# Kernel optimization log

Measured on AMD Instinct MI355X. Metric: run time of the kernel, lower is better.

## Reference

```python
import jax, jax.numpy as jnp
import numpy as np

N, E, D, R, L = 50000, 600000, 64, 65, 2


def setup_inputs() -> dict:
    key = jax.random.key(0)
    ks = jax.random.split(key, 10)
    x = jax.random.normal(ks[0], (N, D), dtype=jnp.float32)
    edge_index = jax.random.randint(ks[1], (2, E), 0, N, dtype=jnp.int64)
    edge_type = jax.random.randint(ks[2], (E,), 0, R, dtype=jnp.int64)
    s = 1.0 / np.sqrt(D)
    W = jax.random.normal(ks[3], (L, R, D, D), dtype=jnp.float32) * s
    root = jax.random.normal(ks[4], (L, D, D), dtype=jnp.float32) * s
    bias = jax.random.normal(ks[5], (L, D), dtype=jnp.float32) * 0.01
    res_W = jax.random.normal(ks[6], (L, D, D), dtype=jnp.float32) * s
    res_b = jax.random.normal(ks[7], (L, D), dtype=jnp.float32) * 0.01
    return {"x": x, "edge_index": edge_index, "edge_type": edge_type,
            "W": W, "root": root, "bias": bias, "res_W": res_W, "res_b": res_b}


def _rgcn_conv(x, src, dst, edge_type, W_r, W_root, b):
    # PyG RGCNConv (num_bases=None, aggr='mean'):
    #   out_i = x_i @ W_root + b + sum_r mean_{j in N_r(i)} (x_j @ W_r)
    # mean is linear, so aggregate raw features per (node, relation) first,
    # then apply the per-relation transform once per node.
    n, d = x.shape
    r = W_r.shape[0]
    seg = dst * r + edge_type                       # [E]
    msg = x[src]                                    # [E, D] gather
    agg = jax.ops.segment_sum(msg, seg, num_segments=n * r).reshape(n, r, d)
    cnt = jax.ops.segment_sum(jnp.ones((msg.shape[0],), x.dtype), seg,
                              num_segments=n * r).reshape(n, r, 1)
    mean = agg / jnp.maximum(cnt, 1.0)              # [N, R, D]
    out = jnp.einsum('nrd,rdk->nk', mean, W_r)
    return out + x @ W_root + b


def reference(x, edge_index, edge_type, W, root, bias, res_W, res_b):
    src, dst = edge_index[0], edge_index[1]
    h = x
    for l in range(W.shape[0]):
        conv = _rgcn_conv(h, src, dst, edge_type, W[l], root[l], bias[l])
        conv = jax.nn.relu(conv)
        # dropout: identity in eval mode
        res = jax.nn.relu(h @ res_W[l] + res_b[l])
        h = conv + res
    return h
```

## Files before the change

kernel.cpp:

```cpp
#include <hip/hip_runtime.h>


constexpr int NN  = 50000;
constexpr int EE  = 600000;
constexpr int DIM = 64;
constexpr int RR  = 65;
constexpr int CHUNK = 256;
constexpr int MAXCHUNKS = EE / CHUNK + RR + 8;
constexpr int SORT_BS = 2048;
constexpr int NSB = (EE + SORT_BS - 1) / SORT_BS;
constexpr int SCAN_BS = 1024;
constexpr int SCAN_NB = (NN + SCAN_BS - 1) / SCAN_BS;
constexpr int XNB = 64;

typedef __attribute__((ext_vector_type(8))) short short8v;
typedef __attribute__((ext_vector_type(4))) float floatx4;

__device__ inline unsigned short f2bf(float f) {
  unsigned int u = __float_as_uint(f);
  return (unsigned short)((u + 0x7fffu + ((u >> 16) & 1u)) >> 16);
}
__device__ inline float bf2f(unsigned short v) {
  return __uint_as_float(((unsigned int)v) << 16);
}


__global__ __launch_bounds__(256) void zero4_k(int4* __restrict__ p, int n4) {
  const int i = blockIdx.x * 256 + threadIdx.x;
  if (i < n4) p[i] = make_int4(0, 0, 0, 0);
}

__global__ __launch_bounds__(512) void cnt_k(const int* __restrict__ dst,
                                             const int* __restrict__ et,
                                             int* __restrict__ cnt, int E) {
  const int e = blockIdx.x * 512 + threadIdx.x;
  if (e < E) atomicAdd(&cnt[et[e] * NN + dst[e]], 1);
}

__global__ __launch_bounds__(512) void bhist_k(const int* __restrict__ et,
                                               int* __restrict__ bhist, int E) {
  __shared__ int lh[RR];
  if (threadIdx.x < RR) lh[threadIdx.x] = 0;
  __syncthreads();
  const int base = blockIdx.x * SORT_BS;
#pragma unroll
  for (int it = 0; it < SORT_BS / 512; ++it) {
    const int e = base + it * 512 + threadIdx.x;
    if (e < E) atomicAdd(&lh[et[e]], 1);
  }
  __syncthreads();
  if (threadIdx.x < RR) bhist[blockIdx.x * RR + threadIdx.x] = lh[threadIdx.x];
}


__global__ __launch_bounds__(1024) void scan1_k(const int* __restrict__ cnt,
                                                int* __restrict__ deg,
                                                int* __restrict__ bsum) {
  __shared__ int s[SCAN_BS];
  const int idx = blockIdx.x * SCAN_BS + threadIdx.x;
  int d = 0;
  if (idx < NN) {
#pragma unroll 13
    for (int r = 0; r < RR; ++r) d += cnt[r * NN + idx];
    deg[idx] = d;
  }
  s[threadIdx.x] = d;
  __syncthreads();
  for (int off = SCAN_BS / 2; off > 0; off >>= 1) {
    if (threadIdx.x < off) s[threadIdx.x] += s[threadIdx.x + off];
    __syncthreads();
  }
  if (threadIdx.x == 0) bsum[blockIdx.x] = s[0];
}

__global__ __launch_bounds__(64) void scan2_k(int* __restrict__ bsum) {
  if (threadIdx.x == 0) {
    int run = 0;
    for (int b = 0; b < SCAN_NB; ++b) { const int v = bsum[b]; bsum[b] = run; run += v; }
  }
}

__global__ __launch_bounds__(1024) void scan3_k(const int* __restrict__ deg,
                                                const int* __restrict__ bsum,
                                                int* __restrict__ rowptr,
                                                int* __restrict__ poscur) {
  __shared__ int s[SCAN_BS];
  const int t = threadIdx.x;
  const int idx = blockIdx.x * SCAN_BS + t;
  const int v = (idx < NN) ? deg[idx] : 0;
  s[t] = v;
  __syncthreads();
  for (int off = 1; off < SCAN_BS; off <<= 1) {
    const int u = (t >= off) ? s[t - off] : 0;
    __syncthreads();
    s[t] += u;
    __syncthreads();
  }
  const int excl = bsum[blockIdx.x] + s[t] - v;
  if (idx < NN) { rowptr[idx] = excl; poscur[idx] = excl; }
  if (idx == NN - 1) rowptr[NN] = EE;
}


__global__ __launch_bounds__(512) void scan_rel_k(const int* __restrict__ bhist,
                                                  int* __restrict__ boffrel,
                                                  int* __restrict__ total) {
  __shared__ int s[512];
  const int r = blockIdx.x;
  const int t = threadIdx.x;
  const int v = (t < NSB) ? bhist[t * RR + r] : 0;
  s[t] = v;
  __syncthreads();
  for (int off = 1; off < 512; off <<= 1) {
    const int u = (t >= off) ? s[t - off] : 0;
    __syncthreads();
    s[t] += u;
    __syncthreads();
  }
  if (t < NSB) boffrel[t * RR + r] = s[t] - v;
  if (t == 511) total[r] = s[511];
}

__global__ __launch_bounds__(128) void scan_tot_k(const int* __restrict__ total,
                                                  int* __restrict__ tptrg,
                                                  int4* __restrict__ chunkArr,
                                                  int* __restrict__ nchunks) {
  __shared__ int tptr[RR + 1], chbase[RR + 1];
  const int t = threadIdx.x;
  if (t == 0) {
    int run = 0, crun = 0;
    for (int r = 0; r < RR; ++r) {
      tptr[r] = run;    run  += total[r];
      chbase[r] = crun; crun += (total[r] + CHUNK - 1) / CHUNK;
    }
    tptr[RR] = run; chbase[RR] = crun;
    *nchunks = crun;
  }
  __syncthreads();
  if (t < RR) {
    tptrg[t] = tptr[t];
    const int tot = total[t];
    const int nc = (tot + CHUNK - 1) / CHUNK;
    for (int i = 0; i < nc; ++i) {
      const int beg = tptr[t] + i * CHUNK;
      chunkArr[chbase[t] + i] = make_int4(beg, min(beg + CHUNK, tptr[t] + tot), t, 0);
    }
  }
}

__global__ __launch_bounds__(512) void scatter_k(const int* __restrict__ src,
                                                 const int* __restrict__ dst,
                                                 const int* __restrict__ et,
                                                 const int* __restrict__ cnt,
                                                 const int* __restrict__ boffrel,
                                                 const int* __restrict__ tptrg,
                                                 int* __restrict__ poscur,
                                                 int* __restrict__ osrc,
                                                 int* __restrict__ opos,
                                                 float* __restrict__ oscale, int E) {
  __shared__ int cur[RR];
  if (threadIdx.x < RR)
    cur[threadIdx.x] = tptrg[threadIdx.x] + boffrel[blockIdx.x * RR + threadIdx.x];
  __syncthreads();
  const int base = blockIdx.x * SORT_BS;
#pragma unroll
  for (int it = 0; it < SORT_BS / 512; ++it) {
    const int e = base + it * 512 + threadIdx.x;
    if (e < E) {
      const int s = src[e], d = dst[e], r = et[e];
      const int q = atomicAdd(&cur[r], 1);
      const int p = atomicAdd(&poscur[d], 1);
      osrc[q] = s;
      opos[q] = p;
      oscale[q] = 1.0f / (float)cnt[r * NN + d];
    }
  }
}


__global__ __launch_bounds__(256) void cvtw_k(const float* __restrict__ W,
                                              unsigned short* __restrict__ WT) {
  const int tid = blockIdx.x * 256 + threadIdx.x;
  const int total4 = 2 * RR * DIM * DIM / 4;
  if (tid >= total4) return;
  const int base = tid * 4;
  const int mat = base >> 12;
  const int rem = base & 4095;
  const int k = rem >> 6, c0 = rem & 63;
  const float4 v = *reinterpret_cast<const float4*>(W + base);
  unsigned short* o = WT + (size_t)mat * 4096;
  o[(c0 + 0) * 64 + k] = f2bf(v.x);
  o[(c0 + 1) * 64 + k] = f2bf(v.y);
  o[(c0 + 2) * 64 + k] = f2bf(v.z);
  o[(c0 + 3) * 64 + k] = f2bf(v.w);
}


__global__ __launch_bounds__(256) void msgm_k(const unsigned short* __restrict__ hbf,
                                              const int* __restrict__ osrc,
                                              const int* __restrict__ opos,
                                              const float* __restrict__ oscale,
                                              const unsigned short* __restrict__ WT,
                                              const int4* __restrict__ chunkArr,
                                              const int* __restrict__ nchunks,
                                              unsigned short* __restrict__ m) {
  const int ci = blockIdx.x;
  if (ci >= *nchunks) return;
  const int4 c = chunkArr[ci];
  const int beg = c.x, end = c.y, rel = c.z;

  __shared__ unsigned short Wl[DIM][72];
  {
    const float4* s4 = reinterpret_cast<const float4*>(WT + (size_t)rel * 4096);
#pragma unroll
    for (int it = 0; it < 2; ++it) {
      const int seg = threadIdx.x + it * 256;
      const int row = seg >> 3, s8 = seg & 7;
      *reinterpret_cast<float4*>(&Wl[row][s8 * 8]) = s4[seg];
    }
  }
  __syncthreads();

  const int w  = threadIdx.x >> 6;
  const int l  = threadIdx.x & 63;
  const int lr = l & 15, lq = l >> 4;

  const int ebase = beg + w * 64;
  if (ebase >= end) return;

  short8v a[4][2];
#pragma unroll
  for (int ct = 0; ct < 4; ++ct)
#pragma unroll
    for (int kk = 0; kk < 2; ++kk)
      a[ct][kk] = *reinterpret_cast<const short8v*>(&Wl[ct * 16 + lr][kk * 32 + lq * 8]);

  short8v b[4][2];
  int eidx[4];
#pragma unroll
  for (int et = 0; et < 4; ++et) {
    eidx[et] = ebase + et * 16 + lr;
    const int e = min(eidx[et], end - 1);
    const int s = osrc[e];
    const unsigned short* hp = hbf + (size_t)s * DIM;
    b[et][0] = *reinterpret_cast<const short8v*>(hp + lq * 8);
    b[et][1] = *reinterpret_cast<const short8v*>(hp + 32 + lq * 8);
  }

  floatx4 acc[4][4];
#pragma unroll
  for (int ct = 0; ct < 4; ++ct)
#pragma unroll
    for (int et = 0; et < 4; ++et)
      acc[ct][et] = (floatx4){0.f, 0.f, 0.f, 0.f};

#pragma unroll
  for (int kk = 0; kk < 2; ++kk)
#pragma unroll
    for (int ct = 0; ct < 4; ++ct)
#pragma unroll
      for (int et = 0; et < 4; ++et)
        acc[ct][et] = __builtin_amdgcn_mfma_f32_16x16x32_bf16(a[ct][kk], b[et][kk],
                                                              acc[ct][et], 0, 0, 0);

#pragma unroll
  for (int et = 0; et < 4; ++et) {
    const int e = eidx[et];
    if (e < end) {
      const float sc = oscale[e];
      unsigned short* op = m + (size_t)opos[e] * DIM;
#pragma unroll
      for (int ct = 0; ct < 4; ++ct) {
        ushort4 o;
        o.x = f2bf(acc[ct][et][0] * sc);
        o.y = f2bf(acc[ct][et][1] * sc);
        o.z = f2bf(acc[ct][et][2] * sc);
        o.w = f2bf(acc[ct][et][3] * sc);
        *reinterpret_cast<ushort4*>(op + ct * 16 + lq * 4) = o;
      }
    }
  }
}

__global__ __launch_bounds__(256) void xform_k(const float* __restrict__ h,
                                               const float* __restrict__ root,
                                               const float* __restrict__ bias,
                                               const float* __restrict__ rw,
                                               const float* __restrict__ rb,
                                               float* __restrict__ rt,
                                               float* __restrict__ rs,
                                               unsigned short* __restrict__ hbf, int N) {
  __shared__ float Wl0[DIM * DIM];
  __shared__ float Wl1[DIM * DIM];
  __shared__ float xs[XNB][68];
#pragma unroll
  for (int i = 0; i < 4; ++i) {
    reinterpret_cast<float4*>(Wl0)[threadIdx.x + i * 256] =
        reinterpret_cast<const float4*>(root)[threadIdx.x + i * 256];
    reinterpret_cast<float4*>(Wl1)[threadIdx.x + i * 256] =
        reinterpret_cast<const float4*>(rw)[threadIdx.x + i * 256];
  }

  const int g = threadIdx.x >> 4, li = threadIdx.x & 15;
  const int base = blockIdx.x * XNB;
#pragma unroll
  for (int r = 0; r < 4; ++r) {
    const int n = base + g * 4 + r;
    float4 v = make_float4(0.f, 0.f, 0.f, 0.f);
    if (n < N) v = *reinterpret_cast<const float4*>(h + (size_t)n * DIM + li * 4);
    *reinterpret_cast<float4*>(&xs[g * 4 + r][li * 4]) = v;
  }
  __syncthreads();

  if (hbf != nullptr) {
#pragma unroll
    for (int r = 0; r < 4; ++r) {
      const int n = base + g * 4 + r;
      if (n < N) {
        const float4 v = *reinterpret_cast<const float4*>(&xs[g * 4 + r][li * 4]);
        ushort4 o;
        o.x = f2bf(v.x); o.y = f2bf(v.y); o.z = f2bf(v.z); o.w = f2bf(v.w);
        *reinterpret_cast<ushort4*>(hbf + (size_t)n * DIM + li * 4) = o;
      }
    }
  }

  float aR[4][4], aS[4][4];
#pragma unroll
  for (int r = 0; r < 4; ++r)
#pragma unroll
    for (int q = 0; q < 4; ++q) { aR[r][q] = 0.f; aS[r][q] = 0.f; }

#pragma unroll 4
  for (int k = 0; k < DIM; ++k) {
    const float4 wr = *reinterpret_cast<const float4*>(&Wl0[k * DIM + li * 4]);
    const float4 wv = *reinterpret_cast<const float4*>(&Wl1[k * DIM + li * 4]);
#pragma unroll
    for (int r = 0; r < 4; ++r) {
      const float xv = xs[g * 4 + r][k];
      aR[r][0] += xv * wr.x; aR[r][1] += xv * wr.y; aR[r][2] += xv * wr.z; aR[r][3] += xv * wr.w;
      aS[r][0] += xv * wv.x; aS[r][1] += xv * wv.y; aS[r][2] += xv * wv.z; aS[r][3] += xv * wv.w;
    }
  }

  const float4 bv = reinterpret_cast<const float4*>(bias)[li];
  const float4 cv = reinterpret_cast<const float4*>(rb)[li];
#pragma unroll
  for (int r = 0; r < 4; ++r) {
    const int n = base + g * 4 + r;
    if (n < N) {
      *reinterpret_cast<float4*>(rt + (size_t)n * DIM + li * 4) =
          make_float4(aR[r][0] + bv.x, aR[r][1] + bv.y, aR[r][2] + bv.z, aR[r][3] + bv.w);
      *reinterpret_cast<float4*>(rs + (size_t)n * DIM + li * 4) =
          make_float4(fmaxf(aS[r][0] + cv.x, 0.f), fmaxf(aS[r][1] + cv.y, 0.f),
                      fmaxf(aS[r][2] + cv.z, 0.f), fmaxf(aS[r][3] + cv.w, 0.f));
    }
  }
}

__global__ __launch_bounds__(256) void gather2_k(const unsigned short* __restrict__ m,
                                                 const int* __restrict__ rowptr,
                                                 const float* __restrict__ rt,
                                                 const float* __restrict__ rs,
                                                 float* __restrict__ hout, int N) {
  const int g = threadIdx.x >> 4, li = threadIdx.x & 15;
  const int n = blockIdx.x * 16 + g;
  if (n >= N) return;

  float a0 = 0.f, a1 = 0.f, a2 = 0.f, a3 = 0.f;
  const int jb = rowptr[n], je = rowptr[n + 1];
  int j = jb;
  for (; j + 4 <= je; j += 4) {
    const ushort4 v0 = *reinterpret_cast<const ushort4*>(m + (size_t)(j + 0) * DIM + li * 4);
    const ushort4 v1 = *reinterpret_cast<const ushort4*>(m + (size_t)(j + 1) * DIM + li * 4);
    const ushort4 v2 = *reinterpret_cast<const ushort4*>(m + (size_t)(j + 2) * DIM + li * 4);
    const ushort4 v3 = *reinterpret_cast<const ushort4*>(m + (size_t)(j + 3) * DIM + li * 4);
    a0 += bf2f(v0.x) + bf2f(v1.x) + bf2f(v2.x) + bf2f(v3.x);
    a1 += bf2f(v0.y) + bf2f(v1.y) + bf2f(v2.y) + bf2f(v3.y);
    a2 += bf2f(v0.z) + bf2f(v1.z) + bf2f(v2.z) + bf2f(v3.z);
    a3 += bf2f(v0.w) + bf2f(v1.w) + bf2f(v2.w) + bf2f(v3.w);
  }
  for (; j < je; ++j) {
    const ushort4 v = *reinterpret_cast<const ushort4*>(m + (size_t)j * DIM + li * 4);
    a0 += bf2f(v.x); a1 += bf2f(v.y); a2 += bf2f(v.z); a3 += bf2f(v.w);
  }

  const float4 t = *reinterpret_cast<const float4*>(rt + (size_t)n * DIM + li * 4);
  const float4 s = *reinterpret_cast<const float4*>(rs + (size_t)n * DIM + li * 4);
  *reinterpret_cast<float4*>(hout + (size_t)n * DIM + li * 4) =
      make_float4(fmaxf(a0 + t.x, 0.f) + s.x, fmaxf(a1 + t.y, 0.f) + s.y,
                  fmaxf(a2 + t.z, 0.f) + s.z, fmaxf(a3 + t.w, 0.f) + s.w);
}


__global__ __launch_bounds__(256) void count_k(const int* __restrict__ dst,
                                               const int* __restrict__ et,
                                               int* __restrict__ cnt, int E) {
  int e = blockIdx.x * 256 + threadIdx.x;
  if (e < E) atomicAdd(&cnt[dst[e] * RR + et[e]], 1);
}

__global__ __launch_bounds__(256) void edge_k(const float* __restrict__ h,
                                              const int* __restrict__ src,
                                              const int* __restrict__ dst,
                                              const int* __restrict__ et,
                                              const float* __restrict__ W,
                                              const int* __restrict__ cnt,
                                              float* __restrict__ accum, int E) {
  __shared__ float xs[16][68];
  const int g = threadIdx.x >> 4, li = threadIdx.x & 15;
  const int e = blockIdx.x * 16 + g;
  if (e >= E) return;
  const int s = src[e], d = dst[e], t = et[e];
  *reinterpret_cast<float4*>(&xs[g][li * 4]) =
      *reinterpret_cast<const float4*>(h + (size_t)s * DIM + li * 4);
  const float* Wt = W + (size_t)t * (DIM * DIM) + li * 4;
  float a0 = 0.f, a1 = 0.f, a2 = 0.f, a3 = 0.f;
#pragma unroll 8
  for (int k = 0; k < DIM; ++k) {
    const float xd = xs[g][k];
    const float4 w = *reinterpret_cast<const float4*>(Wt + k * DIM);
    a0 += xd * w.x; a1 += xd * w.y; a2 += xd * w.z; a3 += xd * w.w;
  }
  const float sc = 1.0f / (float)cnt[d * RR + t];
  float* o = accum + (size_t)d * DIM + li * 4;
  unsafeAtomicAdd(o + 0, a0 * sc);
  unsafeAtomicAdd(o + 1, a1 * sc);
  unsafeAtomicAdd(o + 2, a2 * sc);
  unsafeAtomicAdd(o + 3, a3 * sc);
}

__global__ __launch_bounds__(256) void node_k(const float* __restrict__ h,
                                              const float* __restrict__ root,
                                              const float* __restrict__ bias,
                                              const float* __restrict__ rw,
                                              const float* __restrict__ rb,
                                              float* __restrict__ io, int N) {
  __shared__ float xs[16][68];
  const int g = threadIdx.x >> 4, li = threadIdx.x & 15;
  const int n = blockIdx.x * 16 + g;
  if (n >= N) return;
  *reinterpret_cast<float4*>(&xs[g][li * 4]) =
      *reinterpret_cast<const float4*>(h + (size_t)n * DIM + li * 4);
  float r0 = 0.f, r1 = 0.f, r2 = 0.f, r3 = 0.f;
  float s0 = 0.f, s1 = 0.f, s2 = 0.f, s3 = 0.f;
#pragma unroll 8
  for (int k = 0; k < DIM; ++k) {
    const float hd = xs[g][k];
    const float4 w = *reinterpret_cast<const float4*>(root + k * DIM + li * 4);
    const float4 v = *reinterpret_cast<const float4*>(rw + k * DIM + li * 4);
    r0 += hd * w.x; r1 += hd * w.y; r2 += hd * w.z; r3 += hd * w.w;
    s0 += hd * v.x; s1 += hd * v.y; s2 += hd * v.z; s3 += hd * v.w;
  }
  float* o = io + (size_t)n * DIM + li * 4;
  const float4 acc = *reinterpret_cast<const float4*>(o);
  const float4 b = *reinterpret_cast<const float4*>(bias + li * 4);
  const float4 c = *reinterpret_cast<const float4*>(rb + li * 4);
  float o0 = fmaxf(acc.x + r0 + b.x, 0.f) + fmaxf(s0 + c.x, 0.f);
  float o1 = fmaxf(acc.y + r1 + b.y, 0.f) + fmaxf(s1 + c.y, 0.f);
  float o2 = fmaxf(acc.z + r2 + b.z, 0.f) + fmaxf(s2 + c.z, 0.f);
  float o3 = fmaxf(acc.w + r3 + b.w, 0.f) + fmaxf(s3 + c.w, 0.f);
  *reinterpret_cast<float4*>(o) = make_float4(o0, o1, o2, o3);
}


extern "C" void kernel_launch(void* const* d_in, const int* in_sizes, int n_in,
                              void* d_out, int out_size, void* d_ws, size_t ws_size,
                              hipStream_t stream) {
  const float* x    = (const float*)d_in[0];
  const int*   ei   = (const int*)d_in[1];
  const int*   et   = (const int*)d_in[2];
  const float* W    = (const float*)d_in[3];
  const float* root = (const float*)d_in[4];
  const float* bias = (const float*)d_in[5];
  const float* resW = (const float*)d_in[6];
  const float* resb = (const float*)d_in[7];
  float* out = (float*)d_out;

  const int* src = ei;
  const int* dstp = ei + EE;

  char* ws = (char*)d_ws;
  size_t off = 0;
  auto take = [&](size_t bytes) -> void* {
    void* p = ws + off;
    off = (off + bytes + 255) & ~(size_t)255;
    return p;
  };
  unsigned short* m = (unsigned short*)take((size_t)EE * DIM * sizeof(unsigned short));
  float* h1      = (float*)take((size_t)NN * DIM * sizeof(float));
  int* deg       = (int*)take((size_t)NN * sizeof(int));
  int* rowptr    = (int*)take((size_t)(NN + 1) * sizeof(int));
  int* poscur    = (int*)take((size_t)NN * sizeof(int));
  int* bhist     = (int*)take((size_t)NSB * RR * sizeof(int));
  int* boffrel   = (int*)take((size_t)NSB * RR * sizeof(int));
  int* total     = (int*)take((size_t)RR * sizeof(int));
  int* tptrg     = (int*)take((size_t)RR * sizeof(int));
  int* bsum      = (int*)take((size_t)SCAN_NB * sizeof(int));
  int* osrc      = (int*)take((size_t)EE * sizeof(int));
  int* opos      = (int*)take((size_t)EE * sizeof(int));
  float* oscale  = (float*)take((size_t)EE * sizeof(float));
  int4* chunkArr = (int4*)take((size_t)MAXCHUNKS * sizeof(int4));
  int* nchunks   = (int*)take(256);
  float* rt      = (float*)take((size_t)NN * DIM * sizeof(float));
  float* rs      = (float*)take((size_t)NN * DIM * sizeof(float));
  unsigned short* hbf = (unsigned short*)take((size_t)NN * DIM * sizeof(unsigned short));
  unsigned short* wbt = (unsigned short*)take((size_t)2 * RR * DIM * DIM * sizeof(unsigned short));
  const size_t main_off = off;
  int* cnt       = (int*)m;

  if (main_off <= ws_size) {
    zero4_k<<<(NN * RR / 4 + 255) / 256, 256, 0, stream>>>((int4*)cnt, NN * RR / 4);
    cnt_k<<<(EE + 511) / 512, 512, 0, stream>>>(dstp, et, cnt, EE);
    bhist_k<<<NSB, 512, 0, stream>>>(et, bhist, EE);
    scan1_k<<<SCAN_NB, 1024, 0, stream>>>(cnt, deg, bsum);
    scan2_k<<<1, 64, 0, stream>>>(bsum);
    scan3_k<<<SCAN_NB, 1024, 0, stream>>>(deg, bsum, rowptr, poscur);
    scan_rel_k<<<RR, 512, 0, stream>>>(bhist, boffrel, total);
    scan_tot_k<<<1, 128, 0, stream>>>(total, tptrg, chunkArr, nchunks);
    scatter_k<<<NSB, 512, 0, stream>>>(src, dstp, et, cnt, boffrel, tptrg, poscur,
                                       osrc, opos, oscale, EE);
    cvtw_k<<<(2 * RR * DIM * DIM / 4 + 255) / 256, 256, 0, stream>>>(W, wbt);

    const int XG = (NN + XNB - 1) / XNB;
    xform_k<<<XG, 256, 0, stream>>>(x, root, bias, resW, resb, rt, rs, hbf, NN);
    msgm_k<<<MAXCHUNKS, 256, 0, stream>>>(hbf, osrc, opos, oscale, wbt, chunkArr, nchunks, m);
    gather2_k<<<(NN + 15) / 16, 256, 0, stream>>>(m, rowptr, rt, rs, h1, NN);
    xform_k<<<XG, 256, 0, stream>>>(h1, root + DIM * DIM, bias + DIM,
                                    resW + DIM * DIM, resb + DIM, rt, rs, hbf, NN);
    msgm_k<<<MAXCHUNKS, 256, 0, stream>>>(hbf, osrc, opos, oscale,
                                          wbt + (size_t)RR * DIM * DIM, chunkArr, nchunks, m);
    gather2_k<<<(NN + 15) / 16, 256, 0, stream>>>(m, rowptr, rt, rs, out, NN);
  } else {
    int* fcnt = (int*)ws;
    float* fh1 = (float*)(ws + (size_t)NN * RR * sizeof(int));
    hipMemsetAsync(fcnt, 0, (size_t)NN * RR * sizeof(int), stream);
    hipMemsetAsync(fh1, 0, (size_t)NN * DIM * sizeof(float), stream);
    hipMemsetAsync(out, 0, (size_t)NN * DIM * sizeof(float), stream);
    count_k<<<(EE + 255) / 256, 256, 0, stream>>>(dstp, et, fcnt, EE);
    edge_k<<<(EE + 15) / 16, 256, 0, stream>>>(x, src, dstp, et, W, fcnt, fh1, EE);
    node_k<<<(NN + 15) / 16, 256, 0, stream>>>(x, root, bias, resW, resb, fh1, NN);
    edge_k<<<(EE + 15) / 16, 256, 0, stream>>>(fh1, src, dstp, et,
                                               W + (size_t)RR * DIM * DIM, fcnt, out, EE);
    node_k<<<(NN + 15) / 16, 256, 0, stream>>>(fh1, root + DIM * DIM, bias + DIM,
                                               resW + DIM * DIM, resb + DIM, out, NN);
  }
}
```

Before: 246.3 us.

## Pack counts into 16-bit, fuse histogram kernels, enlarge message chunks and unroll gather

Merges the per-(relation,node) count kernel into the block histogram kernel and stores counts as packed 16-bit halves updated by shifted 32-bit atomics, halving the zeroing and count-read traffic and removing a launch. The serial block-sum scan becomes a wavefront shuffle scan. The message kernel uses 512-edge chunks with 512 threads, loading the weight tile in a single pass, and the gather loop is unrolled by 8 to put more loads in flight. Risks include 16-bit count overflow for very high-degree segments, and the message kernel body (not fully visible) must handle the larger chunk with the new thread count.

```diff
diff --git a/kernel.cpp b/kernel.cpp
--- a/kernel.cpp
+++ b/kernel.cpp
@@ -5,8 +5,8 @@
 constexpr int EE  = 600000;
 constexpr int DIM = 64;
 constexpr int RR  = 65;
-constexpr int CHUNK = 256;
-constexpr int MAXCHUNKS = EE / CHUNK + RR + 8;
+constexpr int MCHUNK = 512;
+constexpr int MAXCHUNKS = EE / MCHUNK + RR + 8;
 constexpr int SORT_BS = 2048;
 constexpr int NSB = (EE + SORT_BS - 1) / SORT_BS;
 constexpr int SCAN_BS = 1024;
@@ -30,15 +30,10 @@
   if (i < n4) p[i] = make_int4(0, 0, 0, 0);
 }
 
-__global__ __launch_bounds__(512) void cnt_k(const int* __restrict__ dst,
-                                             const int* __restrict__ et,
-                                             int* __restrict__ cnt, int E) {
-  const int e = blockIdx.x * 512 + threadIdx.x;
-  if (e < E) atomicAdd(&cnt[et[e] * NN + dst[e]], 1);
-}
-
-__global__ __launch_bounds__(512) void bhist_k(const int* __restrict__ et,
-                                               int* __restrict__ bhist, int E) {
+__global__ __launch_bounds__(512) void hist_k(const int* __restrict__ dst,
+                                              const int* __restrict__ et,
+                                              unsigned int* __restrict__ cnt32,
+                                              int* __restrict__ bhist, int E) {
   __shared__ int lh[RR];
   if (threadIdx.x < RR) lh[threadIdx.x] = 0;
   __syncthreads();
@@ -46,14 +41,19 @@
 #pragma unroll
   for (int it = 0; it < SORT_BS / 512; ++it) {
     const int e = base + it * 512 + threadIdx.x;
-    if (e < E) atomicAdd(&lh[et[e]], 1);
+    if (e < E) {
+      const int d = dst[e], r = et[e];
+      const int c = r * NN + d;
+      atomicAdd(&cnt32[c >> 1], 1u << (16 * (c & 1)));
+      atomicAdd(&lh[r], 1);
+    }
   }
   __syncthreads();
   if (threadIdx.x < RR) bhist[blockIdx.x * RR + threadIdx.x] = lh[threadIdx.x];
 }
 
 
-__global__ __launch_bounds__(1024) void scan1_k(const int* __restrict__ cnt,
+__global__ __launch_bounds__(1024) void scan1_k(const unsigned short* __restrict__ c16,
                                                 int* __restrict__ deg,
                                                 int* __restrict__ bsum) {
   __shared__ int s[SCAN_BS];
@@ -61,7 +61,7 @@
   int d = 0;
   if (idx < NN) {
 #pragma unroll 13
-    for (int r = 0; r < RR; ++r) d += cnt[r * NN + idx];
+    for (int r = 0; r < RR; ++r) d += c16[r * NN + idx];
     deg[idx] = d;
   }
   s[threadIdx.x] = d;
@@ -74,10 +74,14 @@
 }
 
 __global__ __launch_bounds__(64) void scan2_k(int* __restrict__ bsum) {
-  if (threadIdx.x == 0) {
-    int run = 0;
-    for (int b = 0; b < SCAN_NB; ++b) { const int v = bsum[b]; bsum[b] = run; run += v; }
-  }
+  const int t = threadIdx.x;
+  int v = (t < SCAN_NB) ? bsum[t] : 0;
+  const int orig = v;
+  for (int off = 1; off < 64; off <<= 1) {
+    const int u = __shfl_up(v, off, 64);
+    if (t >= off) v += u;
+  }
+  if (t < SCAN_NB) bsum[t] = v - orig;
 }
 
 __global__ __launch_bounds__(1024) void scan3_k(const int* __restrict__ deg,
@@ -131,7 +135,7 @@
     int run = 0, crun = 0;
     for (int r = 0; r < RR; ++r) {
       tptr[r] = run;    run  += total[r];
-      chbase[r] = crun; crun += (total[r] + CHUNK - 1) / CHUNK;
+      chbase[r] = crun; crun += (total[r] + MCHUNK - 1) / MCHUNK;
     }
     tptr[RR] = run; chbase[RR] = crun;
     *nchunks = crun;
@@ -140,10 +144,10 @@
   if (t < RR) {
     tptrg[t] = tptr[t];
     const int tot = total[t];
-    const int nc = (tot + CHUNK - 1) / CHUNK;
+    const int nc = (tot + MCHUNK - 1) / MCHUNK;
     for (int i = 0; i < nc; ++i) {
-      const int beg = tptr[t] + i * CHUNK;
-      chunkArr[chbase[t] + i] = make_int4(beg, min(beg + CHUNK, tptr[t] + tot), t, 0);
+      const int beg = tptr[t] + i * MCHUNK;
+      chunkArr[chbase[t] + i] = make_int4(beg, min(beg + MCHUNK, tptr[t] + tot), t, 0);
     }
   }
 }
@@ -151,7 +155,7 @@
 __global__ __launch_bounds__(512) void scatter_k(const int* __restrict__ src,
                                                  const int* __restrict__ dst,
                                                  const int* __restrict__ et,
-                                                 const int* __restrict__ cnt,
+                                                 const unsigned short* __restrict__ c16,
                                                  const int* __restrict__ boffrel,
                                                  const int* __restrict__ tptrg,
                                                  int* __restrict__ poscur,
@@ -172,7 +176,7 @@
       const int p = atomicAdd(&poscur[d], 1);
       osrc[q] = s;
       opos[q] = p;
-      oscale[q] = 1.0f / (float)cnt[r * NN + d];
+      oscale[q] = 1.0f / (float)c16[r * NN + d];
     }
   }
 }
@@ -196,7 +200,7 @@
 }
 
 
-__global__ __launch_bounds__(256) void msgm_k(const unsigned short* __restrict__ hbf,
+__global__ __launch_bounds__(512) void msgm_k(const unsigned short* __restrict__ hbf,
                                               const int* __restrict__ osrc,
                                               const int* __restrict__ opos,
                                               const float* __restrict__ oscale,
@@ -212,12 +216,9 @@
   __shared__ unsigned short Wl[DIM][72];
   {
     const float4* s4 = reinterpret_cast<const float4*>(WT + (size_t)rel * 4096);
-#pragma unroll
-    for (int it = 0; it < 2; ++it) {
-      const int seg = threadIdx.x + it * 256;
-      const int row = seg >> 3, s8 = seg & 7;
-      *reinterpret_cast<float4*>(&Wl[row][s8 * 8]) = s4[seg];
-    }
+    const int seg = threadIdx.x;
+    const int row = seg >> 3, s8 = seg & 7;
+    *reinterpret_cast<float4*>(&Wl[row][s8 * 8]) = s4[seg];
   }
   __syncthreads();
 
@@ -370,15 +371,25 @@
   float a0 = 0.f, a1 = 0.f, a2 = 0.f, a3 = 0.f;
   const int jb = rowptr[n], je = rowptr[n + 1];
   int j = jb;
+  for (; j + 8 <= je; j += 8) {
+    ushort4 v[8];
+#pragma unroll
+    for (int u = 0; u < 8; ++u)
+      v[u] = *reinterpret_cast<const ushort4*>(m + (size_t)(j + u) * DIM + li * 4);
+#pragma unroll
+    for (int u = 0; u < 8; ++u) {
+      a0 += bf2f(v[u].x); a1 += bf2f(v[u].y); a2 += bf2f(v[u].z); a3 += bf2f(v[u].w);
+    }
+  }
   for (; j + 4 <= je; j += 4) {
-    const ushort4 v0 = *reinterpret_cast<const ushort4*>(m + (size_t)(j + 0) * DIM + li * 4);
-    const ushort4 v1 = *reinterpret_cast<const ushort4*>(m + (size_t)(j + 1) * DIM + li * 4);
-    const ushort4 v2 = *reinterpret_cast<const ushort4*>(m + (size_t)(j + 2) * DIM + li * 4);
-    const ushort4 v3 = *reinterpret_cast<const ushort4*>(m + (size_t)(j + 3) * DIM + li * 4);
-    a0 += bf2f(v0.x) + bf2f(v1.x) + bf2f(v2.x) + bf2f(v3.x);
-    a1 += bf2f(v0.y) + bf2f(v1.y) + bf2f(v2.y) + bf2f(v3.y);
-    a2 += bf2f(v0.z) + bf2f(v1.z) + bf2f(v2.z) + bf2f(v3.z);
-    a3 += bf2f(v0.w) + bf2f(v1.w) + bf2f(v2.w) + bf2f(v3.w);
+    ushort4 v[4];
+#pragma unroll
+    for (int u = 0; u < 4; ++u)
+      v[u] = *reinterpret_cast<const ushort4*>(m + (size_t)(j + u) * DIM + li * 4);
+#pragma unroll
+    for (int u = 0; u < 4; ++u) {
+      a0 += bf2f(v[u].x); a1 += bf2f(v[u].y); a2 += bf2f(v[u].z); a3 += bf2f(v[u].w);
+    }
   }
   for (; j < je; ++j) {
     const ushort4 v = *reinterpret_cast<const ushort4*>(m + (size_t)j * DIM + li * 4);
@@ -507,28 +518,28 @@
   unsigned short* hbf = (unsigned short*)take((size_t)NN * DIM * sizeof(unsigned short));
   unsigned short* wbt = (unsigned short*)take((size_t)2 * RR * DIM * DIM * sizeof(unsigned short));
   const size_t main_off = off;
-  int* cnt       = (int*)m;
+  unsigned int* cnt32 = (unsigned int*)m;
+  const unsigned short* c16 = (const unsigned short*)m;
 
   if (main_off <= ws_size) {
-    zero4_k<<<(NN * RR / 4 + 255) / 256, 256, 0, stream>>>((int4*)cnt, NN * RR / 4);
-    cnt_k<<<(EE + 511) / 512, 512, 0, stream>>>(dstp, et, cnt, EE);
-    bhist_k<<<NSB, 512, 0, stream>>>(et, bhist, EE);
-    scan1_k<<<SCAN_NB, 1024, 0, stream>>>(cnt, deg, bsum);
+    zero4_k<<<(NN * RR * 2 / 16 + 255) / 256, 256, 0, stream>>>((int4*)cnt32, NN * RR * 2 / 16);
+    hist_k<<<NSB, 512, 0, stream>>>(dstp, et, cnt32, bhist, EE);
+    scan1_k<<<SCAN_NB, 1024, 0, stream>>>(c16, deg, bsum);
     scan2_k<<<1, 64, 0, stream>>>(bsum);
     scan3_k<<<SCAN_NB, 1024, 0, stream>>>(deg, bsum, rowptr, poscur);
     scan_rel_k<<<RR, 512, 0, stream>>>(bhist, boffrel, total);
     scan_tot_k<<<1, 128, 0, stream>>>(total, tptrg, chunkArr, nchunks);
-    scatter_k<<<NSB, 512, 0, stream>>>(src, dstp, et, cnt, boffrel, tptrg, poscur,
+    scatter_k<<<NSB, 512, 0, stream>>>(src, dstp, et, c16, boffrel, tptrg, poscur,
                                        osrc, opos, oscale, EE);
     cvtw_k<<<(2 * RR * DIM * DIM / 4 + 255) / 256, 256, 0, stream>>>(W, wbt);
 
     const int XG = (NN + XNB - 1) / XNB;
     xform_k<<<XG, 256, 0, stream>>>(x, root, bias, resW, resb, rt, rs, hbf, NN);
-    msgm_k<<<MAXCHUNKS, 256, 0, stream>>>(hbf, osrc, opos, oscale, wbt, chunkArr, nchunks, m);
+    msgm_k<<<MAXCHUNKS, 512, 0, stream>>>(hbf, osrc, opos, oscale, wbt, chunkArr, nchunks, m);
     gather2_k<<<(NN + 15) / 16, 256, 0, stream>>>(m, rowptr, rt, rs, h1, NN);
     xform_k<<<XG, 256, 0, stream>>>(h1, root + DIM * DIM, bias + DIM,
                                     resW + DIM * DIM, resb + DIM, rt, rs, hbf, NN);
-    msgm_k<<<MAXCHUNKS, 256, 0, stream>>>(hbf, osrc, opos, oscale,
+    msgm_k<<<MAXCHUNKS, 512, 0, stream>>>(hbf, osrc, opos, oscale,
                                           wbt + (size_t)RR * DIM * DIM, chunkArr, nchunks, m);
     gather2_k<<<(NN + 15) / 16, 256, 0, stream>>>(m, rowptr, rt, rs, out, NN);
   } else {
```

Result: slower. 251.8 us (+2.2%).
